# Optimization experiments

Measured on AMD Instinct MI355X. Metric: run time of the kernel, lower is better.

The kernel has to match this reference:

```python
import jax, jax.numpy as jnp
import numpy as np

INPUT_SIZE = 512
HIDDEN = 1024
OUT = 4
SEQ = 2048


def setup_inputs() -> dict:
    key = jax.random.key(0)
    ks = jax.random.split(key, 12)
    s_in = 1.0 / np.sqrt(INPUT_SIZE)
    s_h = 1.0 / np.sqrt(HIDDEN)
    inp = {
        "x": jax.random.normal(ks[0], (SEQ, INPUT_SIZE), jnp.float32),
        "h0": jnp.zeros((1, 1, HIDDEN), jnp.float32),
        "c0": jnp.zeros((1, 1, HIDDEN), jnp.float32),
        # LSTM params (PyTorch layout: gates ordered i, f, g, o along 4H)
        "w_ih": jax.random.uniform(ks[1], (4 * HIDDEN, INPUT_SIZE), jnp.float32, -s_h, s_h),
        "w_hh": jax.random.uniform(ks[2], (4 * HIDDEN, HIDDEN), jnp.float32, -s_h, s_h),
        "b_ih": jax.random.uniform(ks[3], (4 * HIDDEN,), jnp.float32, -s_h, s_h),
        "b_hh": jax.random.uniform(ks[4], (4 * HIDDEN,), jnp.float32, -s_h, s_h),
        "fc1_w": jax.random.uniform(ks[5], (HIDDEN, HIDDEN), jnp.float32, -s_h, s_h),
        "fc1_b": jax.random.uniform(ks[6], (HIDDEN,), jnp.float32, -s_h, s_h),
        "fc2_w": jax.random.uniform(ks[7], (HIDDEN, HIDDEN), jnp.float32, -s_h, s_h),
        "fc2_b": jax.random.uniform(ks[8], (HIDDEN,), jnp.float32, -s_h, s_h),
        "mean_w": jax.random.uniform(ks[9], (OUT, HIDDEN), jnp.float32, -s_h, s_h),
        "mean_b": jax.random.uniform(ks[10], (OUT,), jnp.float32, -s_h, s_h),
        "log_std": jnp.zeros((OUT,), jnp.float32),
    }
    return inp


def _lstm(x, h0, c0, w_ih, w_hh, b_ih, b_hh):
    # Precompute input projections for all timesteps: [T, 4H]
    gx = x @ w_ih.T + b_ih + b_hh
    H = h0.shape[-1]

    def step(carry, gx_t):
        h, c = carry  # [H], [H]
        g = gx_t + h @ w_hh.T  # [4H]
        i = jax.nn.sigmoid(g[0 * H:1 * H])
        f = jax.nn.sigmoid(g[1 * H:2 * H])
        gg = jnp.tanh(g[2 * H:3 * H])
        o = jax.nn.sigmoid(g[3 * H:4 * H])
        c_new = f * c + i * gg
        h_new = o * jnp.tanh(c_new)
        return (h_new, c_new), h_new

    (hT, cT), ys = jax.lax.scan(step, (h0[0, 0], c0[0, 0]), gx)
    return ys, hT[None, None, :], cT[None, None, :]  # ys: [T, H]


def reference(x, h0, c0, w_ih, w_hh, b_ih, b_hh, fc1_w, fc1_b, fc2_w, fc2_b, mean_w, mean_b, log_std):
    ys, hT, cT = _lstm(x, h0, c0, w_ih, w_hh, b_ih, b_hh)
    h1 = jax.nn.relu(ys @ fc1_w.T + fc1_b)
    h2 = jax.nn.relu(h1 @ fc2_w.T + fc2_b)
    action_mean = h2 @ mean_w.T + mean_b  # [T, OUT]
    action_log_std = jnp.broadcast_to(log_std, action_mean.shape)
    return action_mean, action_log_std, hT, cT
```

## Files before the change

### kernel.cpp

```cpp
#include <hip/hip_runtime.h>
#include <stdint.h>


#define T_SEQ 2048
#define H 1024
#define G4 4096
#define K_IN 512
#define SENT 0x7FC0DEADu

__device__ __forceinline__ float sigmoidf_(float x) { return 1.0f / (1.0f + __expf(-x)); }
__device__ __forceinline__ float tanhf_(float x) { return 1.0f - 2.0f / (1.0f + __expf(2.0f * x)); }

__global__ void init_k(const float* __restrict__ h0, float* __restrict__ h_hist) {
  int idx = blockIdx.x * blockDim.x + threadIdx.x;
  if (idx < H) {
    h_hist[idx] = h0[idx];
  } else if (idx < (T_SEQ + 1) * H) {
    ((unsigned*)h_hist)[idx] = SENT;
  }
}

#define BM 64
#define BN 64
#define BK 32
#define LDT 68

template <bool RELU, bool HASB2>
__global__ __launch_bounds__(256) void gemm_bias_k(
    const float* __restrict__ A, const float* __restrict__ Bw,
    const float* __restrict__ b1, const float* __restrict__ b2,
    float* __restrict__ C, int M, int N, int K) {
  __shared__ float As[BK][LDT];
  __shared__ float Bs[BK][LDT];
  const int tid = threadIdx.x;
  const int m0 = blockIdx.y * BM;
  const int n0 = blockIdx.x * BN;
  const int tx = tid & 15, ty = tid >> 4;
  const int srow = tid >> 2;
  const int skq = tid & 3;

  float acc[4][4];
#pragma unroll
  for (int i = 0; i < 4; i++)
#pragma unroll
    for (int j = 0; j < 4; j++) acc[i][j] = 0.f;

  const float* Arow = A + (size_t)(m0 + srow) * K;
  const float* Brow = Bw + (size_t)(n0 + srow) * K;

  for (int k0 = 0; k0 < K; k0 += BK) {
    float4 a0 = *(const float4*)(Arow + k0 + skq * 8);
    float4 a1 = *(const float4*)(Arow + k0 + skq * 8 + 4);
    float4 c0_ = *(const float4*)(Brow + k0 + skq * 8);
    float4 c1_ = *(const float4*)(Brow + k0 + skq * 8 + 4);
    __syncthreads();
    const int kb = skq * 8;
    As[kb + 0][srow] = a0.x; As[kb + 1][srow] = a0.y; As[kb + 2][srow] = a0.z; As[kb + 3][srow] = a0.w;
    As[kb + 4][srow] = a1.x; As[kb + 5][srow] = a1.y; As[kb + 6][srow] = a1.z; As[kb + 7][srow] = a1.w;
    Bs[kb + 0][srow] = c0_.x; Bs[kb + 1][srow] = c0_.y; Bs[kb + 2][srow] = c0_.z; Bs[kb + 3][srow] = c0_.w;
    Bs[kb + 4][srow] = c1_.x; Bs[kb + 5][srow] = c1_.y; Bs[kb + 6][srow] = c1_.z; Bs[kb + 7][srow] = c1_.w;
    __syncthreads();
#pragma unroll
    for (int kk = 0; kk < BK; kk++) {
      float av[4], bv[4];
      *(float4*)av = *(const float4*)&As[kk][ty * 4];
      *(float4*)bv = *(const float4*)&Bs[kk][tx * 4];
#pragma unroll
      for (int i = 0; i < 4; i++)
#pragma unroll
        for (int j = 0; j < 4; j++) acc[i][j] = fmaf(av[i], bv[j], acc[i][j]);
    }
  }

  float bb[4];
#pragma unroll
  for (int j = 0; j < 4; j++) {
    bb[j] = b1[n0 + tx * 4 + j];
    if (HASB2) bb[j] += b2[n0 + tx * 4 + j];
  }
#pragma unroll
  for (int i = 0; i < 4; i++) {
    float4 o;
    float* op = (float*)&o;
#pragma unroll
    for (int j = 0; j < 4; j++) {
      float v = acc[i][j] + bb[j];
      op[j] = RELU ? fmaxf(v, 0.f) : v;
    }
    *(float4*)&C[(size_t)(m0 + ty * 4 + i) * N + n0 + tx * 4] = o;
  }
}

#define NWG 256
#define NTHR 256
#define HPAD 68

__global__ __launch_bounds__(NTHR) void lstm_k(
    const float* __restrict__ gx, const float* __restrict__ w_hh,
    const float* __restrict__ c0, float* __restrict__ h_hist,
    float* __restrict__ out) {
  unsigned* h_u = (unsigned*)h_hist;
  __shared__ float hbuf[2][16 * HPAD];
  const int tid = threadIdx.x;
  const int wg = blockIdx.x;
  const int wave = tid >> 6, lane = tid & 63;
  const int g = lane & 3;
  const int s = lane >> 2;
  const int unit = wg * 4 + wave;
  const int grow = g * 1024 + unit;

  float wreg[64];
  {
    const float* wp = w_hh + (size_t)grow * H + s * 64;
#pragma unroll
    for (int j = 0; j < 64; j += 4) {
      float4 w4 = *(const float4*)(wp + j);
      wreg[j] = w4.x; wreg[j + 1] = w4.y; wreg[j + 2] = w4.z; wreg[j + 3] = w4.w;
    }
#pragma unroll
    for (int j = 0; j < 64; j++) asm volatile("" : "+v"(wreg[j]));
  }
  float c = c0[unit];

  const int stage_idx = 4 * tid + (tid >> 4) * 4;
  for (int t = 0; t < T_SEQ; t++) {
    const int buf = t & 1;
    float gxv = gx[(size_t)t * G4 + grow];
    asm volatile("" : "+v"(gxv));

    {
      uint64_t* src = (uint64_t*)(h_u + (size_t)t * H) + tid * 2;
      uint64_t a = __hip_atomic_load(&src[0], __ATOMIC_RELAXED, __HIP_MEMORY_SCOPE_AGENT);
      uint64_t b = __hip_atomic_load(&src[1], __ATOMIC_RELAXED, __HIP_MEMORY_SCOPE_AGENT);
      while ((unsigned)a == SENT || (unsigned)(a >> 32) == SENT)
        a = __hip_atomic_load(&src[0], __ATOMIC_RELAXED, __HIP_MEMORY_SCOPE_AGENT);
      while ((unsigned)b == SENT || (unsigned)(b >> 32) == SENT)
        b = __hip_atomic_load(&src[1], __ATOMIC_RELAXED, __HIP_MEMORY_SCOPE_AGENT);
      float4 v;
      v.x = __uint_as_float((unsigned)a);
      v.y = __uint_as_float((unsigned)(a >> 32));
      v.z = __uint_as_float((unsigned)b);
      v.w = __uint_as_float((unsigned)(b >> 32));
      *(float4*)&hbuf[buf][stage_idx] = v;
    }
    __syncthreads();

    float acc0 = 0.f, acc1 = 0.f, acc2 = 0.f, acc3 = 0.f;
    const float* hs = &hbuf[buf][s * HPAD];
#pragma unroll
    for (int j = 0; j < 16; j++) {
      float4 hv = *(const float4*)(hs + j * 4);
      acc0 = fmaf(wreg[4 * j + 0], hv.x, acc0);
      acc1 = fmaf(wreg[4 * j + 1], hv.y, acc1);
      acc2 = fmaf(wreg[4 * j + 2], hv.z, acc2);
      acc3 = fmaf(wreg[4 * j + 3], hv.w, acc3);
    }
    float accv = (acc0 + acc1) + (acc2 + acc3);
    accv += __shfl_xor(accv, 4);
    accv += __shfl_xor(accv, 8);
    accv += __shfl_xor(accv, 16);
    accv += __shfl_xor(accv, 32);
    float pre = accv + gxv;
    float act = (g == 2) ? tanhf_(pre) : sigmoidf_(pre);
    float b1v = __shfl_xor(act, 1);
    float b2v = __shfl_xor(act, 2);
    float b3v = __shfl_xor(act, 3);
    c = fmaf(b1v, c, act * b2v);
    float hn = b3v * tanhf_(c);
    if (lane == 0) {
      __hip_atomic_store(&h_u[(size_t)(t + 1) * H + unit], __float_as_uint(hn),
                         __ATOMIC_RELAXED, __HIP_MEMORY_SCOPE_AGENT);
      if (t == T_SEQ - 1) {
        out[16384 + unit] = hn;
        out[17408 + unit] = c;
      }
    }
  }
}

__global__ __launch_bounds__(256) void head_k(
    const float* __restrict__ h2, const float* __restrict__ mean_w,
    const float* __restrict__ mean_b, const float* __restrict__ log_std,
    float* __restrict__ out) {
  const int t = blockIdx.x;
  const int tid = threadIdx.x;
  const int wave = tid >> 6, lane = tid & 63;
  const float* hr = h2 + (size_t)t * H;
  const float* wr = mean_w + (size_t)wave * H;
  float s = 0.f;
#pragma unroll
  for (int j = 0; j < 16; j++) s = fmaf(hr[lane + j * 64], wr[lane + j * 64], s);
#pragma unroll
  for (int off = 32; off > 0; off >>= 1) s += __shfl_down(s, off);
  if (lane == 0) out[t * 4 + wave] = s + mean_b[wave];
  if (tid < 4) out[8192 + t * 4 + tid] = log_std[tid];
}

extern "C" void kernel_launch(void* const* d_in, const int* in_sizes, int n_in,
                              void* d_out, int out_size, void* d_ws, size_t ws_size,
                              hipStream_t stream) {
  const float* x      = (const float*)d_in[0];
  const float* h0     = (const float*)d_in[1];
  const float* c0     = (const float*)d_in[2];
  const float* w_ih   = (const float*)d_in[3];
  const float* w_hh   = (const float*)d_in[4];
  const float* b_ih   = (const float*)d_in[5];
  const float* b_hh   = (const float*)d_in[6];
  const float* fc1_w  = (const float*)d_in[7];
  const float* fc1_b  = (const float*)d_in[8];
  const float* fc2_w  = (const float*)d_in[9];
  const float* fc2_b  = (const float*)d_in[10];
  const float* mean_w = (const float*)d_in[11];
  const float* mean_b = (const float*)d_in[12];
  const float* lstd   = (const float*)d_in[13];
  float* out = (float*)d_out;

  float* gx = (float*)d_ws;
  float* h_hist = gx + (size_t)T_SEQ * G4;
  float* h1 = gx;
  float* h2 = gx + (size_t)T_SEQ * H;

  init_k<<<dim3((T_SEQ + 1) * H / 256), 256, 0, stream>>>(h0, h_hist);
  gemm_bias_k<false, true><<<dim3(G4 / BN, T_SEQ / BM), 256, 0, stream>>>(
      x, w_ih, b_ih, b_hh, gx, T_SEQ, G4, K_IN);
  lstm_k<<<dim3(NWG), NTHR, 0, stream>>>(gx, w_hh, c0, h_hist, out);
  gemm_bias_k<true, false><<<dim3(H / BN, T_SEQ / BM), 256, 0, stream>>>(
      h_hist + H, fc1_w, fc1_b, nullptr, h1, T_SEQ, H, H);
  gemm_bias_k<true, false><<<dim3(H / BN, T_SEQ / BM), 256, 0, stream>>>(
      h1, fc2_w, fc2_b, nullptr, h2, T_SEQ, H, H);
  head_k<<<dim3(T_SEQ), 256, 0, stream>>>(h2, mean_w, mean_b, lstd, out);
}
```

Measured before the change: 4.772 ms.

## Use 128 persistent LSTM workgroups of 512 threads with 16-byte coherent polling

Halves the number of persistent LSTM workgroups by packing eight hidden units per 512-thread block, so fewer blocks each poll the full hidden-state vector every timestep. Only the first 256 threads poll, using a single 16-byte global load with sc0 sc1 cache bypass bits instead of two 64-bit atomic loads. This cuts global polling traffic and cross-CU contention on the recurrent barrier. In exchange, each block now holds more register-resident weights and there are fewer blocks spread across the GPU. The inline-asm load's coherence relies on the cache-bypass bits.

```diff
diff --git a/kernel.cpp b/kernel.cpp
--- a/kernel.cpp
+++ b/kernel.cpp
@@ -10,6 +10,13 @@
 
 __device__ __forceinline__ float sigmoidf_(float x) { return 1.0f / (1.0f + __expf(-x)); }
 __device__ __forceinline__ float tanhf_(float x) { return 1.0f - 2.0f / (1.0f + __expf(2.0f * x)); }
+
+__device__ __forceinline__ uint4 poll_load16(const uint4* p) {
+  uint4 v;
+  asm volatile("global_load_dwordx4 %0, %1, off sc0 sc1\n\ts_waitcnt vmcnt(0)"
+               : "=v"(v) : "v"(p) : "memory");
+  return v;
+}
 
 __global__ void init_k(const float* __restrict__ h0, float* __restrict__ h_hist) {
   int idx = blockIdx.x * blockDim.x + threadIdx.x;
@@ -91,11 +98,11 @@
   }
 }
 
-#define NWG 256
-#define NTHR 256
+#define NWG 128
+#define NTHR 512
 #define HPAD 68
 
-__global__ __launch_bounds__(NTHR) void lstm_k(
+__global__ __launch_bounds__(NTHR, 2) void lstm_k(
     const float* __restrict__ gx, const float* __restrict__ w_hh,
     const float* __restrict__ c0, float* __restrict__ h_hist,
     float* __restrict__ out) {
@@ -106,7 +113,7 @@
   const int wave = tid >> 6, lane = tid & 63;
   const int g = lane & 3;
   const int s = lane >> 2;
-  const int unit = wg * 4 + wave;
+  const int unit = wg * 8 + wave;
   const int grow = g * 1024 + unit;
 
   float wreg[64];
@@ -122,26 +129,23 @@
   }
   float c = c0[unit];
 
+  const bool poller = tid < 256;
   const int stage_idx = 4 * tid + (tid >> 4) * 4;
+
   for (int t = 0; t < T_SEQ; t++) {
     const int buf = t & 1;
     float gxv = gx[(size_t)t * G4 + grow];
     asm volatile("" : "+v"(gxv));
 
-    {
-      uint64_t* src = (uint64_t*)(h_u + (size_t)t * H) + tid * 2;
-      uint64_t a = __hip_atomic_load(&src[0], __ATOMIC_RELAXED, __HIP_MEMORY_SCOPE_AGENT);
-      uint64_t b = __hip_atomic_load(&src[1], __ATOMIC_RELAXED, __HIP_MEMORY_SCOPE_AGENT);
-      while ((unsigned)a == SENT || (unsigned)(a >> 32) == SENT)
-        a = __hip_atomic_load(&src[0], __ATOMIC_RELAXED, __HIP_MEMORY_SCOPE_AGENT);
-      while ((unsigned)b == SENT || (unsigned)(b >> 32) == SENT)
-        b = __hip_atomic_load(&src[1], __ATOMIC_RELAXED, __HIP_MEMORY_SCOPE_AGENT);
-      float4 v;
-      v.x = __uint_as_float((unsigned)a);
-      v.y = __uint_as_float((unsigned)(a >> 32));
-      v.z = __uint_as_float((unsigned)b);
-      v.w = __uint_as_float((unsigned)(b >> 32));
-      *(float4*)&hbuf[buf][stage_idx] = v;
+    if (poller) {
+      const uint4* src = (const uint4*)(h_u + (size_t)t * H) + tid;
+      uint4 v = poll_load16(src);
+      while (v.x == SENT || v.y == SENT || v.z == SENT || v.w == SENT)
+        v = poll_load16(src);
+      float4 f;
+      f.x = __uint_as_float(v.x); f.y = __uint_as_float(v.y);
+      f.z = __uint_as_float(v.z); f.w = __uint_as_float(v.w);
+      *(float4*)&hbuf[buf][stage_idx] = f;
     }
     __syncthreads();
 
```

Result: faster. 3.944 ms (-17.3%).
